# Performance work log

Hardware: AMD Instinct MI355X
Metric: run time of the kernel (lower is better)

Reference implementation:

```python
import jax, jax.numpy as jnp
import numpy as np

B, S, D = 8, 2048, 512  # batch, seq_len, d_model (= units*heads = 64*8)


def setup_inputs() -> dict:
    key = jax.random.key(0)
    k1, k2, k3, k4 = jax.random.split(key, 4)
    scale = 1.0 / np.sqrt(D)
    return {
        "data": jax.random.normal(k1, (B, S, D), dtype=jnp.float32),
        "Wq": jax.random.normal(k2, (D, D), dtype=jnp.float32) * scale,
        "Wk": jax.random.normal(k3, (D, D), dtype=jnp.float32) * scale,
        "Wv": jax.random.normal(k4, (D, D), dtype=jnp.float32) * scale,
    }


def reference(data, Wq, Wk, Wv):
    # Bias-free projections (no head split in the original module).
    q = data @ Wq  # [B,S,D]
    k = data @ Wk
    v = data @ Wv
    scores = jnp.einsum("bsd,btd->bst", q, k)  # [B,S,S]
    # NOTE: original scales by sqrt(weight.shape[-1]) == sqrt(seq_len), not sqrt(d_k).
    scores = scores / jnp.sqrt(jnp.float32(scores.shape[-1]))
    # Causal mask: (w + 1e6) * tril - 1e6  ==  where(tril, w, -1e6)
    causal = jnp.tril(jnp.ones((scores.shape[1], scores.shape[2]), dtype=bool))
    scores = jnp.where(causal[None, :, :], scores, jnp.float32(-1e6))
    attn = jax.nn.softmax(scores, axis=-1)
    return jnp.einsum("bst,btd->bsd", attn, v)  # [B,S,D]
```

## Files before the change

### kernel.cpp

```cpp
#include <hip/hip_runtime.h>

typedef unsigned short u16;
typedef __attribute__((ext_vector_type(8))) short short8;
typedef __attribute__((ext_vector_type(4))) float f32x4;


__device__ __forceinline__ u16 f2bf(float f) {
    unsigned u = __float_as_uint(f);
    u += 0x7fffu + ((u >> 16) & 1u);
    return (u16)(u >> 16);
}

__device__ __forceinline__ void lds_cp16(const u16* g, u16* l) {
#if defined(__has_builtin) && __has_builtin(__builtin_amdgcn_global_load_lds)
    __builtin_amdgcn_global_load_lds(
        (const __attribute__((address_space(1))) void*)g,
        (__attribute__((address_space(3))) void*)l, 16, 0, 0);
#else
    *(uint4*)l = *(const uint4*)g;
#endif
}

template <bool ROWSUM>
__device__ __forceinline__ void gemm_core(const u16* __restrict__ Ag, int lda,
                                          const u16* __restrict__ Bg, int ldb,
                                          int ksteps, u16* Alds, u16* Blds,
                                          f32x4 (&acc)[4][4], f32x4* accL) {
    const int t = threadIdx.x;
    const int lane = t & 63;
    const int w = t >> 6;
    const int wr = (w >> 1) * 64;
    const int wc = (w & 1) * 64;
    const short8* A8 = (const short8*)Alds;
    const short8* B8 = (const short8*)Blds;
    const short ob = (short)0x3f80;
    const short8 ones = {ob, ob, ob, ob, ob, ob, ob, ob};

    for (int kt = 0; kt < ksteps; ++kt) {
        __syncthreads();
#pragma unroll
        for (int p = 0; p < 2; ++p) {
            const int el = w * 512 + lane * 8 + p * 2048;
            const int row = el >> 5, col = el & 31;
            lds_cp16(Ag + (size_t)row * lda + kt * 32 + col, Alds + el);
            lds_cp16(Bg + (size_t)row * ldb + kt * 32 + col, Blds + el);
        }
        __syncthreads();

        short8 a[4], b[4];
#pragma unroll
        for (int i = 0; i < 4; ++i)
            a[i] = A8[(wr + i * 16 + (lane & 15)) * 4 + (lane >> 4)];
#pragma unroll
        for (int j = 0; j < 4; ++j)
            b[j] = B8[(wc + j * 16 + (lane & 15)) * 4 + (lane >> 4)];
#pragma unroll
        for (int i = 0; i < 4; ++i)
#pragma unroll
            for (int j = 0; j < 4; ++j)
                acc[i][j] = __builtin_amdgcn_mfma_f32_16x16x32_bf16(a[i], b[j], acc[i][j], 0, 0, 0);
        if constexpr (ROWSUM) {
#pragma unroll
            for (int i = 0; i < 4; ++i)
                accL[i] = __builtin_amdgcn_mfma_f32_16x16x32_bf16(a[i], ones, accL[i], 0, 0, 0);
        }
    }
}


__global__ void k_cvt_x(const float4* __restrict__ X, ushort4* __restrict__ Xb, int n4) {
    for (int i = blockIdx.x * blockDim.x + threadIdx.x; i < n4; i += gridDim.x * blockDim.x) {
        float4 v = X[i];
        ushort4 o;
        o.x = f2bf(v.x); o.y = f2bf(v.y); o.z = f2bf(v.z); o.w = f2bf(v.w);
        Xb[i] = o;
    }
}

__global__ void k_cvt_w(const float* __restrict__ Wq, const float* __restrict__ Wk,
                        const float* __restrict__ Wv, u16* __restrict__ Wt) {
    int idx = blockIdx.x * 256 + threadIdx.x;
    int z = idx >> 18;
    int nk = idx & 262143;
    int n = nk >> 9, k = nk & 511;
    const float* W = (z == 0) ? Wq : (z == 1 ? Wk : Wv);
    float v = W[k * 512 + n];
    if (z == 0) v *= 0.022097086912079608f;
    Wt[idx] = f2bf(v);
}

__global__ __launch_bounds__(256, 2) void k_proj(const u16* __restrict__ Xb, const u16* __restrict__ Wt,
                                                 u16* __restrict__ Qb, u16* __restrict__ Kb,
                                                 u16* __restrict__ Vt) {
    __shared__ alignas(16) u16 Alds[4096];
    __shared__ alignas(16) u16 Blds[4096];
    const int bid = blockIdx.x;
    const int u = bid >> 3;
    const int z = u >> 6;
    const int nt = (u >> 4) & 3;
    const int mt = (bid & 7) * 16 + (u & 15);
    const u16* Ag = Xb + (size_t)mt * 128 * 512;
    const u16* Bg = Wt + (size_t)z * 512 * 512 + (size_t)nt * 128 * 512;
    f32x4 acc[4][4] = {};
    gemm_core<false>(Ag, 512, Bg, 512, 16, Alds, Blds, acc, (f32x4*)nullptr);

    const int t = threadIdx.x, lane = t & 63, w = t >> 6;
    const int wr = (w >> 1) * 64, wc = (w & 1) * 64;
    if (z < 2) {
        u16* O = (z == 0) ? Qb : Kb;
#pragma unroll
        for (int i = 0; i < 4; ++i)
#pragma unroll
            for (int j = 0; j < 4; ++j)
#pragma unroll
                for (int r = 0; r < 4; ++r) {
                    int m = mt * 128 + wr + i * 16 + 4 * (lane >> 4) + r;
                    int n = nt * 128 + wc + j * 16 + (lane & 15);
                    O[(size_t)m * 512 + n] = f2bf(acc[i][j][r]);
                }
    } else {
        int b = mt >> 4;
#pragma unroll
        for (int i = 0; i < 4; ++i)
#pragma unroll
            for (int j = 0; j < 4; ++j) {
                int s0 = (mt * 128 + wr + i * 16 + 4 * (lane >> 4)) & 2047;
                int d = nt * 128 + wc + j * 16 + (lane & 15);
                ushort4 pk;
                pk.x = f2bf(acc[i][j][0]); pk.y = f2bf(acc[i][j][1]);
                pk.z = f2bf(acc[i][j][2]); pk.w = f2bf(acc[i][j][3]);
                *(ushort4*)(Vt + (size_t)b * 512 * 2048 + (size_t)d * 2048 + s0) = pk;
            }
    }
}

__global__ __launch_bounds__(256, 2) void k_scores(const u16* __restrict__ Qb, const u16* __restrict__ Kb,
                                                   u16* __restrict__ P) {
    const int bid = blockIdx.x;
    const int bz = bid & 7;
    const int tt = bid >> 3;
    int qi = (int)((sqrtf(8.0f * tt + 1.0f) - 1.0f) * 0.5f);
    while ((qi + 1) * (qi + 2) / 2 <= tt) ++qi;
    while (qi * (qi + 1) / 2 > tt) --qi;
    const int kvj = tt - qi * (qi + 1) / 2;

    __shared__ alignas(16) u16 Alds[4096];
    __shared__ alignas(16) u16 Blds[4096];
    const u16* Ag = Qb + (size_t)bz * 2048 * 512 + (size_t)qi * 128 * 512;
    const u16* Bg = Kb + (size_t)bz * 2048 * 512 + (size_t)kvj * 128 * 512;
    f32x4 acc[4][4] = {};
    gemm_core<false>(Ag, 512, Bg, 512, 16, Alds, Blds, acc, (f32x4*)nullptr);

    const int t = threadIdx.x, lane = t & 63, w = t >> 6;
    const int wr = (w >> 1) * 64, wc = (w & 1) * 64;
    u16* Pb = P + (size_t)bz * 2048 * 2048;
#pragma unroll
    for (int i = 0; i < 4; ++i)
#pragma unroll
        for (int j = 0; j < 4; ++j)
#pragma unroll
            for (int r = 0; r < 4; ++r) {
                int q = qi * 128 + wr + i * 16 + 4 * (lane >> 4) + r;
                int kv = kvj * 128 + wc + j * 16 + (lane & 15);
                float pv = (kv <= q) ? __expf(acc[i][j][r]) : 0.0f;
                Pb[(size_t)q * 2048 + kv] = f2bf(pv);
            }
}

__global__ __launch_bounds__(256, 2) void k_pv(const u16* __restrict__ P, const u16* __restrict__ Vt,
                                               float* __restrict__ Out) {
    __shared__ alignas(16) u16 Alds[4096];
    __shared__ alignas(16) u16 Blds[4096];
    const int bid = blockIdx.x;
    const int bz = bid & 7;
    const int u = bid >> 3;
    const int h = u & 1;
    const int j2 = u >> 1;
    const int qpair = j2 >> 2;
    const int nt = j2 & 3;
    const int qi = h ? (15 - qpair) : qpair;

    const u16* Ag = P + (size_t)bz * 2048 * 2048 + (size_t)qi * 128 * 2048;
    const u16* Bg = Vt + (size_t)bz * 512 * 2048 + (size_t)nt * 128 * 2048;
    f32x4 acc[4][4] = {};
    f32x4 accL[4] = {};
    gemm_core<true>(Ag, 2048, Bg, 2048, (qi + 1) * 4, Alds, Blds, acc, accL);

    const int t = threadIdx.x, lane = t & 63, w = t >> 6;
    const int wr = (w >> 1) * 64, wc = (w & 1) * 64;
#pragma unroll
    for (int i = 0; i < 4; ++i) {
        float inv[4];
#pragma unroll
        for (int r = 0; r < 4; ++r) inv[r] = 1.0f / accL[i][r];
#pragma unroll
        for (int j = 0; j < 4; ++j) {
            int d = nt * 128 + wc + j * 16 + (lane & 15);
#pragma unroll
            for (int r = 0; r < 4; ++r) {
                int q = qi * 128 + wr + i * 16 + 4 * (lane >> 4) + r;
                Out[(size_t)bz * 2048 * 512 + (size_t)q * 512 + d] = acc[i][j][r] * inv[r];
            }
        }
    }
}


extern "C" void kernel_launch(void* const* d_in, const int* in_sizes, int n_in,
                              void* d_out, int out_size, void* d_ws, size_t ws_size,
                              hipStream_t stream) {
    const float* data = (const float*)d_in[0];
    const float* Wq = (const float*)d_in[1];
    const float* Wk = (const float*)d_in[2];
    const float* Wv = (const float*)d_in[3];
    float* out = (float*)d_out;
    char* ws = (char*)d_ws;

    u16* Xb = (u16*)(ws);
    u16* Qb = (u16*)(ws + 16777216);
    u16* Kb = (u16*)(ws + 33554432);
    u16* Vt = (u16*)(ws + 50331648);
    u16* Wt = (u16*)(ws + 67108864);
    u16* P  = (u16*)(ws + 68681728);

    k_cvt_x<<<2048, 256, 0, stream>>>((const float4*)data, (ushort4*)Xb, (8 * 2048 * 512) / 4);
    k_cvt_w<<<3072, 256, 0, stream>>>(Wq, Wk, Wv, Wt);
    k_proj<<<1536, 256, 0, stream>>>(Xb, Wt, Qb, Kb, Vt);
    k_scores<<<1088, 256, 0, stream>>>(Qb, Kb, P);
    k_pv<<<512, 256, 0, stream>>>(P, Vt, out);
}
```

Baseline: 131.0 us.

## Double-buffer LDS in GEMM core and split PV into 64-row query tiles

```diff
diff --git a/kernel.cpp b/kernel.cpp
--- a/kernel.cpp
+++ b/kernel.cpp
@@ -31,22 +31,27 @@
     const int w = t >> 6;
     const int wr = (w >> 1) * 64;
     const int wc = (w & 1) * 64;
-    const short8* A8 = (const short8*)Alds;
-    const short8* B8 = (const short8*)Blds;
+    const int el0 = t * 8;
     const short ob = (short)0x3f80;
     const short8 ones = {ob, ob, ob, ob, ob, ob, ob, ob};
 
+    auto stage = [&](int kt, int buf) {
+#pragma unroll
+        for (int p = 0; p < 2; ++p) {
+            const int el = el0 + p * 2048;
+            const int row = el >> 5, col = el & 31;
+            lds_cp16(Ag + (size_t)row * lda + kt * 32 + col, Alds + buf * 4096 + el);
+            lds_cp16(Bg + (size_t)row * ldb + kt * 32 + col, Blds + buf * 4096 + el);
+        }
+    };
+
+    stage(0, 0);
+    int cur = 0;
     for (int kt = 0; kt < ksteps; ++kt) {
         __syncthreads();
-#pragma unroll
-        for (int p = 0; p < 2; ++p) {
-            const int el = w * 512 + lane * 8 + p * 2048;
-            const int row = el >> 5, col = el & 31;
-            lds_cp16(Ag + (size_t)row * lda + kt * 32 + col, Alds + el);
-            lds_cp16(Bg + (size_t)row * ldb + kt * 32 + col, Blds + el);
-        }
-        __syncthreads();
-
+        if (kt + 1 < ksteps) stage(kt + 1, cur ^ 1);
+        const short8* A8 = (const short8*)(Alds + cur * 4096);
+        const short8* B8 = (const short8*)(Blds + cur * 4096);
         short8 a[4], b[4];
 #pragma unroll
         for (int i = 0; i < 4; ++i)
@@ -64,6 +69,7 @@
             for (int i = 0; i < 4; ++i)
                 accL[i] = __builtin_amdgcn_mfma_f32_16x16x32_bf16(a[i], ones, accL[i], 0, 0, 0);
         }
+        cur ^= 1;
     }
 }
 
@@ -89,11 +95,11 @@
     Wt[idx] = f2bf(v);
 }
 
-__global__ __launch_bounds__(256, 2) void k_proj(const u16* __restrict__ Xb, const u16* __restrict__ Wt,
+__global__ __launch_bounds__(256, 4) void k_proj(const u16* __restrict__ Xb, const u16* __restrict__ Wt,
                                                  u16* __restrict__ Qb, u16* __restrict__ Kb,
                                                  u16* __restrict__ Vt) {
-    __shared__ alignas(16) u16 Alds[4096];
-    __shared__ alignas(16) u16 Blds[4096];
+    __shared__ alignas(16) u16 Alds[2][4096];
+    __shared__ alignas(16) u16 Blds[2][4096];
     const int bid = blockIdx.x;
     const int u = bid >> 3;
     const int z = u >> 6;
@@ -102,7 +108,7 @@
     const u16* Ag = Xb + (size_t)mt * 128 * 512;
     const u16* Bg = Wt + (size_t)z * 512 * 512 + (size_t)nt * 128 * 512;
     f32x4 acc[4][4] = {};
-    gemm_core<false>(Ag, 512, Bg, 512, 16, Alds, Blds, acc, (f32x4*)nullptr);
+    gemm_core<false>(Ag, 512, Bg, 512, 16, &Alds[0][0], &Blds[0][0], acc, (f32x4*)nullptr);
 
     const int t = threadIdx.x, lane = t & 63, w = t >> 6;
     const int wr = (w >> 1) * 64, wc = (w & 1) * 64;
@@ -134,7 +140,7 @@
     }
 }
 
-__global__ __launch_bounds__(256, 2) void k_scores(const u16* __restrict__ Qb, const u16* __restrict__ Kb,
+__global__ __launch_bounds__(256, 4) void k_scores(const u16* __restrict__ Qb, const u16* __restrict__ Kb,
                                                    u16* __restrict__ P) {
     const int bid = blockIdx.x;
     const int bz = bid & 7;
@@ -144,12 +150,12 @@
     while (qi * (qi + 1) / 2 > tt) --qi;
     const int kvj = tt - qi * (qi + 1) / 2;
 
-    __shared__ alignas(16) u16 Alds[4096];
-    __shared__ alignas(16) u16 Blds[4096];
+    __shared__ alignas(16) u16 Alds[2][4096];
+    __shared__ alignas(16) u16 Blds[2][4096];
     const u16* Ag = Qb + (size_t)bz * 2048 * 512 + (size_t)qi * 128 * 512;
     const u16* Bg = Kb + (size_t)bz * 2048 * 512 + (size_t)kvj * 128 * 512;
     f32x4 acc[4][4] = {};
-    gemm_core<false>(Ag, 512, Bg, 512, 16, Alds, Blds, acc, (f32x4*)nullptr);
+    gemm_core<false>(Ag, 512, Bg, 512, 16, &Alds[0][0], &Blds[0][0], acc, (f32x4*)nullptr);
 
     const int t = threadIdx.x, lane = t & 63, w = t >> 6;
     const int wr = (w >> 1) * 64, wc = (w & 1) * 64;
@@ -167,38 +173,76 @@
             }
 }
 
-__global__ __launch_bounds__(256, 2) void k_pv(const u16* __restrict__ P, const u16* __restrict__ Vt,
+__global__ __launch_bounds__(256, 4) void k_pv(const u16* __restrict__ P, const u16* __restrict__ Vt,
                                                float* __restrict__ Out) {
-    __shared__ alignas(16) u16 Alds[4096];
-    __shared__ alignas(16) u16 Blds[4096];
+    __shared__ alignas(16) u16 Alds[2][2048];
+    __shared__ alignas(16) u16 Blds[2][4096];
     const int bid = blockIdx.x;
     const int bz = bid & 7;
     const int u = bid >> 3;
-    const int h = u & 1;
-    const int j2 = u >> 1;
-    const int qpair = j2 >> 2;
-    const int nt = j2 & 3;
-    const int qi = h ? (15 - qpair) : qpair;
-
-    const u16* Ag = P + (size_t)bz * 2048 * 2048 + (size_t)qi * 128 * 2048;
+    const int g = u >> 5;
+    const int s = u & 31;
+    const int nt = g;
+    const int qi2 = (g & 1) ? (31 - s) : s;
+    const int ksteps = (qi2 + 1) * 2;
+
+    const int t = threadIdx.x, lane = t & 63, w = t >> 6;
+    const int l = lane & 15, g4 = lane >> 4;
+    const int wr = (w >> 1) * 32, wc = (w & 1) * 64;
+    const u16* Ag = P + (size_t)bz * 2048 * 2048 + (size_t)qi2 * 64 * 2048;
     const u16* Bg = Vt + (size_t)bz * 512 * 2048 + (size_t)nt * 128 * 2048;
-    f32x4 acc[4][4] = {};
-    f32x4 accL[4] = {};
-    gemm_core<true>(Ag, 2048, Bg, 2048, (qi + 1) * 4, Alds, Blds, acc, accL);
-
-    const int t = threadIdx.x, lane = t & 63, w = t >> 6;
-    const int wr = (w >> 1) * 64, wc = (w & 1) * 64;
-#pragma unroll
-    for (int i = 0; i < 4; ++i) {
+    const short ob = (short)0x3f80;
+    const short8 ones = {ob, ob, ob, ob, ob, ob, ob, ob};
+
+    auto stage = [&](int kt, int buf) {
+        {
+            const int el = t * 8;
+            const int row = el >> 5, col = el & 31;
+            lds_cp16(Ag + (size_t)row * 2048 + kt * 32 + col, &Alds[buf][el]);
+        }
+#pragma unroll
+        for (int p = 0; p < 2; ++p) {
+            const int el = t * 8 + p * 2048;
+            const int row = el >> 5, col = el & 31;
+            lds_cp16(Bg + (size_t)row * 2048 + kt * 32 + col, &Blds[buf][el]);
+        }
+    };
+
+    f32x4 acc[2][4] = {};
+    f32x4 accL[2] = {};
+    stage(0, 0);
+    int cur = 0;
+    for (int kt = 0; kt < ksteps; ++kt) {
+        __syncthreads();
+        if (kt + 1 < ksteps) stage(kt + 1, cur ^ 1);
+        const short8* A8 = (const short8*)&Alds[cur][0];
+        const short8* B8 = (const short8*)&Blds[cur][0];
+        short8 a[2], b[4];
+#pragma unroll
+        for (int i = 0; i < 2; ++i) a[i] = A8[(wr + i * 16 + l) * 4 + g4];
+#pragma unroll
+        for (int j = 0; j < 4; ++j) b[j] = B8[(wc + j * 16 + l) * 4 + g4];
+#pragma unroll
+        for (int i = 0; i < 2; ++i) {
+#pragma unroll
+            for (int j = 0; j < 4; ++j)
+                acc[i][j] = __builtin_amdgcn_mfma_f32_16x16x32_bf16(a[i], b[j], acc[i][j], 0, 0, 0);
+            accL[i] = __builtin_amdgcn_mfma_f32_16x16x32_bf16(a[i], ones, accL[i], 0, 0, 0);
+        }
+        cur ^= 1;
+    }
+
+#pragma unroll
+    for (int i = 0; i < 2; ++i) {
         float inv[4];
 #pragma unroll
         for (int r = 0; r < 4; ++r) inv[r] = 1.0f / accL[i][r];
 #pragma unroll
         for (int j = 0; j < 4; ++j) {
-            int d = nt * 128 + wc + j * 16 + (lane & 15);
+            const int d = nt * 128 + wc + j * 16 + l;
 #pragma unroll
             for (int r = 0; r < 4; ++r) {
-                int q = qi * 128 + wr + i * 16 + 4 * (lane >> 4) + r;
+                const int q = qi2 * 64 + wr + i * 16 + 4 * g4 + r;
                 Out[(size_t)bz * 2048 * 512 + (size_t)q * 512 + d] = acc[i][j][r] * inv[r];
             }
         }
@@ -227,5 +271,5 @@
     k_cvt_w<<<3072, 256, 0, stream>>>(Wq, Wk, Wv, Wt);
     k_proj<<<1536, 256, 0, stream>>>(Xb, Wt, Qb, Kb, Vt);
     k_scores<<<1088, 256, 0, stream>>>(Qb, Kb, P);
-    k_pv<<<512, 256, 0, stream>>>(P, Vt, out);
-}
+    k_pv<<<1024, 256, 0, stream>>>(P, Vt, out);
+}
```

Result: no change. 131.7 us (+0.6%).
